# Performance work log

Measured on AMD Instinct MI355X. Metric: run time of the kernel, lower is better.

Reference implementation:

```python
import jax, jax.numpy as jnp
import numpy as np

N = 4096  # n_out = n_in = d_in


def setup_inputs() -> dict:
    key = jax.random.key(0)
    ks = jax.random.split(key, 12)
    f = lambda k, shape: jax.random.normal(k, shape, dtype=jnp.float32)
    center = f(ks[10], (N,))
    radius = jnp.abs(f(ks[11], (N,)))
    return dict(
        W=f(ks[0], (N, N)),
        b=f(ks[1], (N,)),
        prev_W_upper=f(ks[2], (N, N)),
        prev_W_lower=f(ks[3], (N, N)),
        prev_b_upper=f(ks[4], (N,)),
        prev_b_lower=f(ks[5], (N,)),
        prev_W_upper2=f(ks[6], (N, N)),
        prev_W_lower2=f(ks[7], (N, N)),
        prev_b_upper2=f(ks[8], (N,)),
        prev_b_lower2=f(ks[9], (N,)),
        prev_ub=center + radius,
        prev_lb=center - radius,
    )


def reference(W, b, prev_W_upper, prev_W_lower, prev_b_upper, prev_b_lower,
              prev_W_upper2, prev_W_lower2, prev_b_upper2, prev_b_lower2,
              prev_ub, prev_lb):
    # torch: (w_pos * W) @ X + (~w_pos * W) @ Y  ->  W+ @ X + W- @ Y
    Wp = jnp.maximum(W, 0.0)  # W * (W >= 0)
    Wm = jnp.minimum(W, 0.0)  # W * (W <  0)

    # --- forward: compose symbolic bounds with prev layer's ---
    W_upper = Wp @ prev_W_upper + Wm @ prev_W_lower            # [N, N]
    b_upper = Wp @ prev_b_upper + Wm @ prev_b_lower + b        # [N]
    W_lower = Wp @ prev_W_lower + Wm @ prev_W_upper
    b_lower = Wp @ prev_b_lower + Wm @ prev_b_upper + b

    # concretize with W_upper2 = W_lower2 = W, b_upper2 = b_lower2 = b
    ub = Wp @ prev_ub + Wm @ prev_lb + b
    lb = Wp @ prev_lb + Wm @ prev_ub + b

    # --- backsub (prev is the input layer, prev.prev = None -> 1 loop iter) ---
    best_ub, best_lb = ub, lb
    # loop iteration: W_upper = W_lower = W, b_upper = b_lower = b
    ub1 = Wp @ prev_ub + Wm @ prev_lb + b
    lb1 = Wp @ prev_lb + Wm @ prev_ub + b
    best_lb = jnp.maximum(best_lb, lb1)
    best_ub = jnp.minimum(best_ub, ub1)
    bu = Wp @ prev_b_upper2 + Wm @ prev_b_lower2 + b
    bl = Wp @ prev_b_lower2 + Wm @ prev_b_upper2 + b
    Wu = Wp @ prev_W_upper2 + Wm @ prev_W_lower2
    Wl = Wp @ prev_W_lower2 + Wm @ prev_W_upper2
    # final block after loop exit (layer = input layer)
    Wup, Wum = jnp.maximum(Wu, 0.0), jnp.minimum(Wu, 0.0)
    Wlp, Wlm = jnp.maximum(Wl, 0.0), jnp.minimum(Wl, 0.0)
    ub2 = Wup @ prev_ub + Wum @ prev_lb + bu
    lb2 = Wlp @ prev_lb + Wlm @ prev_ub + bl
    best_lb = jnp.maximum(best_lb, lb2)
    best_ub = jnp.minimum(best_ub, ub2)

    bounds = jnp.stack([ub, lb, best_ub, best_lb])  # [4, N]
    return (bounds, W_upper, W_lower, b_upper, b_lower)
```

## Files before the change

kernel.cpp:

```cpp
#include <hip/hip_runtime.h>
#include <hip/hip_bf16.h>
#include <stdint.h>

#define NN 4096

typedef __attribute__((ext_vector_type(8))) short   short8;
typedef __attribute__((ext_vector_type(8))) __bf16  bf16x8;
typedef __attribute__((ext_vector_type(4))) float   f32x4;

__device__ __forceinline__ uint16_t f2bf(float f) {
  uint32_t u = __float_as_uint(f);
  u += 0x7fff + ((u >> 16) & 1);
  return (uint16_t)(u >> 16);
}
__device__ __forceinline__ uint32_t pack2(float a, float b) {
  return (uint32_t)f2bf(a) | ((uint32_t)f2bf(b) << 16);
}

__device__ __forceinline__ void gl_lds16(const void* g, void* l) {
  __builtin_amdgcn_global_load_lds(
      (__attribute__((address_space(1))) void*)g,
      (__attribute__((address_space(3))) void*)l, 16, 0, 0);
}

__global__ __launch_bounds__(256)
void tp_sumdiff(const float* __restrict__ X, const float* __restrict__ Y,
                uint16_t* __restrict__ S, uint16_t* __restrict__ D, int jbase) {
  __shared__ uint16_t sS[64][66];
  __shared__ uint16_t sD[64][66];
  const int t   = threadIdx.x;
  const int j0l = blockIdx.x * 64;
  const int k0  = blockIdx.y * 64;
  const int r   = t >> 2;
  const int c   = (t & 3) * 16;
  const size_t goff = (size_t)(k0 + r) * NN + jbase + j0l + c;
  const float4* px = (const float4*)(X + goff);
  const float4* py = (const float4*)(Y + goff);
#pragma unroll
  for (int i = 0; i < 4; ++i) {
    const float4 vx = px[i];
    const float4 vy = py[i];
    sS[r][c + 4*i]     = f2bf(vx.x + vy.x);
    sS[r][c + 4*i + 1] = f2bf(vx.y + vy.y);
    sS[r][c + 4*i + 2] = f2bf(vx.z + vy.z);
    sS[r][c + 4*i + 3] = f2bf(vx.w + vy.w);
    sD[r][c + 4*i]     = f2bf(vx.x - vy.x);
    sD[r][c + 4*i + 1] = f2bf(vx.y - vy.y);
    sD[r][c + 4*i + 2] = f2bf(vx.z - vy.z);
    sD[r][c + 4*i + 3] = f2bf(vx.w - vy.w);
  }
  __syncthreads();
  const int jj = t >> 2;
  const int kc = (t & 3) * 16;
  uint32_t vs[8], vd[8];
#pragma unroll
  for (int i = 0; i < 8; ++i) {
    vs[i] = (uint32_t)sS[kc + 2*i][jj] | ((uint32_t)sS[kc + 2*i + 1][jj] << 16);
    vd[i] = (uint32_t)sD[kc + 2*i][jj] | ((uint32_t)sD[kc + 2*i + 1][jj] << 16);
  }
  const size_t ooff = (size_t)(j0l + jj) * NN + k0 + kc;
  uint4* ps = (uint4*)(S + ooff);
  uint4* pd = (uint4*)(D + ooff);
  ps[0] = make_uint4(vs[0], vs[1], vs[2], vs[3]);
  ps[1] = make_uint4(vs[4], vs[5], vs[6], vs[7]);
  pd[0] = make_uint4(vd[0], vd[1], vd[2], vd[3]);
  pd[1] = make_uint4(vd[4], vd[5], vd[6], vd[7]);
}

__global__ __launch_bounds__(256)
void wcvt(const float* __restrict__ W, uint16_t* __restrict__ Wb) {
  const size_t base = ((size_t)blockIdx.x * 256 + threadIdx.x) * 8;
  const float4 v0 = *(const float4*)(W + base);
  const float4 v1 = *(const float4*)(W + base + 4);
  *(uint4*)(Wb + base) = make_uint4(pack2(v0.x, v0.y), pack2(v0.z, v0.w),
                                    pack2(v1.x, v1.y), pack2(v1.z, v1.w));
}

__device__ __forceinline__ void epi_write(const f32x4 (&accS)[4][4], const f32x4 (&accD)[4][4],
                                          float* __restrict__ outU, float* __restrict__ outL,
                                          int i0, int j0, int jbase,
                                          int wm, int wn, int lr, int q) {
#pragma unroll
  for (int f = 0; f < 4; ++f)
#pragma unroll
    for (int g = 0; g < 4; ++g) {
      const int col = jbase + j0 + wn + g * 16 + lr;
#pragma unroll
      for (int r = 0; r < 4; ++r) {
        const int row = i0 + wm + f * 16 + q * 4 + r;
        const float s = accS[f][g][r], d = accD[f][g][r];
        outU[(size_t)row * NN + col] = (s + d) * 0.5f;
        outL[(size_t)row * NN + col] = (s - d) * 0.5f;
      }
    }
}

__device__ __forceinline__ void epi_reduce(const f32x4 (&accS)[4][4], const f32x4 (&accD)[4][4],
                                           const float* __restrict__ pub, const float* __restrict__ plb,
                                           float* __restrict__ accUv, float* __restrict__ accLv,
                                           int i0, int j0, int jbase,
                                           int wm, int wn, int lr, int q) {
  float uv[4], lv[4];
#pragma unroll
  for (int g = 0; g < 4; ++g) {
    const int col = jbase + j0 + wn + g * 16 + lr;
    uv[g] = pub[col];
    lv[g] = plb[col];
  }
  float su[16], sl[16];
#pragma unroll
  for (int f = 0; f < 4; ++f)
#pragma unroll
    for (int r = 0; r < 4; ++r) {
      float au = 0.f, al = 0.f;
#pragma unroll
      for (int g = 0; g < 4; ++g) {
        const float s  = accS[f][g][r], d = accD[f][g][r];
        const float wu = (s + d) * 0.5f;
        const float wl = (s - d) * 0.5f;
        au += fmaxf(wu, 0.f) * uv[g] + fminf(wu, 0.f) * lv[g];
        al += fmaxf(wl, 0.f) * lv[g] + fminf(wl, 0.f) * uv[g];
      }
      su[f * 4 + r] = au;
      sl[f * 4 + r] = al;
    }
#pragma unroll
  for (int m = 1; m < 16; m <<= 1)
#pragma unroll
    for (int p = 0; p < 16; ++p) {
      su[p] += __shfl_xor(su[p], m, 64);
      sl[p] += __shfl_xor(sl[p], m, 64);
    }
  const int row = i0 + wm + (lr >> 2) * 16 + q * 4 + (lr & 3);
  atomicAdd(&accUv[row], su[lr]);
  atomicAdd(&accLv[row], sl[lr]);
}

template <int MODE>
__global__ __launch_bounds__(256, 2)
void gemm_bf16(const uint16_t* __restrict__ Ab,
               const uint16_t* __restrict__ Bs,
               const uint16_t* __restrict__ Bd,
               float* __restrict__ outU, float* __restrict__ outL,
               const float* __restrict__ pub, const float* __restrict__ plb,
               float* __restrict__ accUv, float* __restrict__ accLv, int jbase) {
  __shared__ __align__(16) uint16_t sA [128 * 32];
  __shared__ __align__(16) uint16_t sBs[128 * 32];
  __shared__ __align__(16) uint16_t sBd[128 * 32];

  const int tid  = threadIdx.x;
  const int lane = tid & 63;
  const int wv   = tid >> 6;
  const int i0   = blockIdx.y * 128;
  const int j0   = blockIdx.x * 128;
  const int wm   = (wv >> 1) * 64;
  const int wn   = (wv & 1) * 64;
  const int lr   = lane & 15;
  const int q    = lane >> 4;

  f32x4 accS[4][4], accD[4][4];
#pragma unroll
  for (int f = 0; f < 4; ++f)
#pragma unroll
    for (int g = 0; g < 4; ++g) {
      accS[f][g] = f32x4{0.f, 0.f, 0.f, 0.f};
      accD[f][g] = f32x4{0.f, 0.f, 0.f, 0.f};
    }

  const int e0 = tid, e1 = tid + 256;
  const size_t gA0 = (size_t)(i0 + (e0 >> 2)) * NN + (e0 & 3) * 8;
  const size_t gA1 = (size_t)(i0 + (e1 >> 2)) * NN + (e1 & 3) * 8;
  const size_t gB0 = (size_t)(j0 + (e0 >> 2)) * NN + (e0 & 3) * 8;
  const size_t gB1 = (size_t)(j0 + (e1 >> 2)) * NN + (e1 & 3) * 8;

  uint16_t* lA0 = sA  + wv * 512;
  uint16_t* lA1 = sA  + 2048 + wv * 512;
  uint16_t* lS0 = sBs + wv * 512;
  uint16_t* lS1 = sBs + 2048 + wv * 512;
  uint16_t* lD0 = sBd + wv * 512;
  uint16_t* lD1 = sBd + 2048 + wv * 512;

  const short8 msk = {0x7fff,0x7fff,0x7fff,0x7fff,0x7fff,0x7fff,0x7fff,0x7fff};

  for (int kk = 0; kk < NN; kk += 32) {
    __syncthreads();
    gl_lds16(Ab + gA0 + kk, lA0);
    gl_lds16(Ab + gA1 + kk, lA1);
    gl_lds16(Bs + gB0 + kk, lS0);
    gl_lds16(Bs + gB1 + kk, lS1);
    gl_lds16(Bd + gB0 + kk, lD0);
    gl_lds16(Bd + gB1 + kk, lD1);
    __syncthreads();

    bf16x8 a[4], aa[4];
#pragma unroll
    for (int f = 0; f < 4; ++f) {
      short8 as = *(const short8*)(sA + (wm + f * 16 + lr) * 32 + q * 8);
      a[f]  = __builtin_bit_cast(bf16x8, as);
      aa[f] = __builtin_bit_cast(bf16x8, (short8)(as & msk));
    }
#pragma unroll
    for (int g = 0; g < 4; ++g) {
      bf16x8 bs = *(const bf16x8*)(sBs + (wn + g * 16 + lr) * 32 + q * 8);
      bf16x8 bd = *(const bf16x8*)(sBd + (wn + g * 16 + lr) * 32 + q * 8);
#pragma unroll
      for (int f = 0; f < 4; ++f) {
        accS[f][g] = __builtin_amdgcn_mfma_f32_16x16x32_bf16(a[f],  bs, accS[f][g], 0, 0, 0);
        accD[f][g] = __builtin_amdgcn_mfma_f32_16x16x32_bf16(aa[f], bd, accD[f][g], 0, 0, 0);
      }
    }
  }

  if (MODE == 0) {
    epi_write(accS, accD, outU, outL, i0, j0, jbase, wm, wn, lr, q);
  } else {
    epi_reduce(accS, accD, pub, plb, accUv, accLv, i0, j0, jbase, wm, wn, lr, q);
  }
}

template <int MODE>
__global__ __launch_bounds__(256, 2)
void gemm_fused(const float* __restrict__ Wg,
                const uint16_t* __restrict__ Bs,
                const uint16_t* __restrict__ Bd,
                float* __restrict__ outU, float* __restrict__ outL,
                const float* __restrict__ pub, const float* __restrict__ plb,
                float* __restrict__ accUv, float* __restrict__ accLv, int jbase) {
  __shared__ __align__(16) uint16_t sA [128 * 32];
  __shared__ __align__(16) uint16_t sBs[128 * 32];
  __shared__ __align__(16) uint16_t sBd[128 * 32];

  const int tid  = threadIdx.x;
  const int lane = tid & 63;
  const int wv   = tid >> 6;
  const int i0   = blockIdx.y * 128;
  const int j0   = blockIdx.x * 128;
  const int wm   = (wv >> 1) * 64;
  const int wn   = (wv & 1) * 64;
  const int lr   = lane & 15;
  const int q    = lane >> 4;

  f32x4 accS[4][4], accD[4][4];
#pragma unroll
  for (int f = 0; f < 4; ++f)
#pragma unroll
    for (int g = 0; g < 4; ++g) {
      accS[f][g] = f32x4{0.f, 0.f, 0.f, 0.f};
      accD[f][g] = f32x4{0.f, 0.f, 0.f, 0.f};
    }

  const int e0 = tid, e1 = tid + 256;
  const size_t ga0 = (size_t)(i0 + (e0 >> 2)) * NN + (e0 & 3) * 8;
  const size_t ga1 = (size_t)(i0 + (e1 >> 2)) * NN + (e1 & 3) * 8;
  const size_t gb0 = (size_t)(j0 + (e0 >> 2)) * NN + (e0 & 3) * 8;
  const size_t gb1 = (size_t)(j0 + (e1 >> 2)) * NN + (e1 & 3) * 8;

  uint16_t* lS0 = sBs + wv * 512;
  uint16_t* lS1 = sBs + 2048 + wv * 512;
  uint16_t* lD0 = sBd + wv * 512;
  uint16_t* lD1 = sBd + 2048 + wv * 512;

  const short8 msk = {0x7fff,0x7fff,0x7fff,0x7fff,0x7fff,0x7fff,0x7fff,0x7fff};

  for (int kk = 0; kk < NN; kk += 32) {
    const float4 a00 = *(const float4*)(Wg + ga0 + kk);
    const float4 a01 = *(const float4*)(Wg + ga0 + kk + 4);
    const float4 a10 = *(const float4*)(Wg + ga1 + kk);
    const float4 a11 = *(const float4*)(Wg + ga1 + kk + 4);
    const uint4 wA0 = make_uint4(pack2(a00.x, a00.y), pack2(a00.z, a00.w),
                                 pack2(a01.x, a01.y), pack2(a01.z, a01.w));
    const uint4 wA1 = make_uint4(pack2(a10.x, a10.y), pack2(a10.z, a10.w),
                                 pack2(a11.x, a11.y), pack2(a11.z, a11.w));
    __syncthreads();
    gl_lds16(Bs + gb0 + kk, lS0);
    gl_lds16(Bs + gb1 + kk, lS1);
    gl_lds16(Bd + gb0 + kk, lD0);
    gl_lds16(Bd + gb1 + kk, lD1);
    *(uint4*)(sA + e0 * 8) = wA0;
    *(uint4*)(sA + e1 * 8) = wA1;
    __syncthreads();

    bf16x8 a[4], aa[4];
#pragma unroll
    for (int f = 0; f < 4; ++f) {
      short8 as = *(const short8*)(sA + (wm + f * 16 + lr) * 32 + q * 8);
      a[f]  = __builtin_bit_cast(bf16x8, as);
      aa[f] = __builtin_bit_cast(bf16x8, (short8)(as & msk));
    }
#pragma unroll
    for (int g = 0; g < 4; ++g) {
      bf16x8 bs = *(const bf16x8*)(sBs + (wn + g * 16 + lr) * 32 + q * 8);
      bf16x8 bd = *(const bf16x8*)(sBd + (wn + g * 16 + lr) * 32 + q * 8);
#pragma unroll
      for (int f = 0; f < 4; ++f) {
        accS[f][g] = __builtin_amdgcn_mfma_f32_16x16x32_bf16(a[f],  bs, accS[f][g], 0, 0, 0);
        accD[f][g] = __builtin_amdgcn_mfma_f32_16x16x32_bf16(aa[f], bd, accD[f][g], 0, 0, 0);
      }
    }
  }

  if (MODE == 0) {
    epi_write(accS, accD, outU, outL, i0, j0, jbase, wm, wn, lr, q);
  } else {
    epi_reduce(accS, accD, pub, plb, accUv, accLv, i0, j0, jbase, wm, wn, lr, q);
  }
}

__device__ __forceinline__ void load16(const float* p, float* f) {
  const float4* q4 = (const float4*)p;
#pragma unroll
  for (int i = 0; i < 4; ++i) {
    const float4 v = q4[i];
    f[4*i] = v.x; f[4*i+1] = v.y; f[4*i+2] = v.z; f[4*i+3] = v.w;
  }
}

__global__ __launch_bounds__(256)
void matvec6(const float* __restrict__ Wg, const float* __restrict__ bvec,
             const float* __restrict__ pbu,  const float* __restrict__ pbl,
             const float* __restrict__ pbu2, const float* __restrict__ pbl2,
             const float* __restrict__ pub,  const float* __restrict__ plb,
             float* __restrict__ out_bu, float* __restrict__ out_bl,
             float* __restrict__ bounds,
             float* __restrict__ bu_f, float* __restrict__ bl_f) {
  const int row = blockIdx.x;
  const int t   = threadIdx.x;
  const int c0  = t * 16;
  float w[16], xu[16], xl[16], x2u[16], x2l[16], uu[16], ul[16];
  load16(Wg + (size_t)row * NN + c0, w);
  load16(pbu  + c0, xu);  load16(pbl  + c0, xl);
  load16(pbu2 + c0, x2u); load16(pbl2 + c0, x2l);
  load16(pub  + c0, uu);  load16(plb  + c0, ul);
  float a_bu = 0, a_bl = 0, a_ub = 0, a_lb = 0, a_2u = 0, a_2l = 0;
#pragma unroll
  for (int i = 0; i < 16; ++i) {
    const float wp = fmaxf(w[i], 0.f), wm = fminf(w[i], 0.f);
    a_bu += wp * xu[i]  + wm * xl[i];
    a_bl += wp * xl[i]  + wm * xu[i];
    a_ub += wp * uu[i]  + wm * ul[i];
    a_lb += wp * ul[i]  + wm * uu[i];
    a_2u += wp * x2u[i] + wm * x2l[i];
    a_2l += wp * x2l[i] + wm * x2u[i];
  }
#pragma unroll
  for (int off = 32; off; off >>= 1) {
    a_bu += __shfl_down(a_bu, off, 64);
    a_bl += __shfl_down(a_bl, off, 64);
    a_ub += __shfl_down(a_ub, off, 64);
    a_lb += __shfl_down(a_lb, off, 64);
    a_2u += __shfl_down(a_2u, off, 64);
    a_2l += __shfl_down(a_2l, off, 64);
  }
  __shared__ float red[4][6];
  const int lane = t & 63, wvv = t >> 6;
  if (lane == 0) {
    red[wvv][0] = a_bu; red[wvv][1] = a_bl; red[wvv][2] = a_ub;
    red[wvv][3] = a_lb; red[wvv][4] = a_2u; red[wvv][5] = a_2l;
  }
  __syncthreads();
  if (t == 0) {
    float r0=0, r1=0, r2=0, r3=0, r4=0, r5=0;
    for (int v = 0; v < 4; ++v) {
      r0 += red[v][0]; r1 += red[v][1]; r2 += red[v][2];
      r3 += red[v][3]; r4 += red[v][4]; r5 += red[v][5];
    }
    const float bb = bvec[row];
    out_bu[row]      = r0 + bb;
    out_bl[row]      = r1 + bb;
    bounds[row]      = r2 + bb;
    bounds[NN + row] = r3 + bb;
    bu_f[row]        = r4 + bb;
    bl_f[row]        = r5 + bb;
  }
}

__global__ __launch_bounds__(256)
void finalize_bounds(const float* __restrict__ accU, const float* __restrict__ accL,
                     const float* __restrict__ bu_f, const float* __restrict__ bl_f,
                     float* __restrict__ bounds) {
  const int i = blockIdx.x * 256 + threadIdx.x;
  if (i >= NN) return;
  const float ub  = bounds[i];
  const float lb  = bounds[NN + i];
  const float ub2 = accU[i] + bu_f[i];
  const float lb2 = accL[i] + bl_f[i];
  bounds[2 * NN + i] = fminf(ub, ub2);
  bounds[3 * NN + i] = fmaxf(lb, lb2);
}

extern "C" void kernel_launch(void* const* d_in, const int* in_sizes, int n_in,
                              void* d_out, int out_size, void* d_ws, size_t ws_size,
                              hipStream_t stream) {
  const float* W    = (const float*)d_in[0];
  const float* b    = (const float*)d_in[1];
  const float* pWu  = (const float*)d_in[2];
  const float* pWl  = (const float*)d_in[3];
  const float* pbu  = (const float*)d_in[4];
  const float* pbl  = (const float*)d_in[5];
  const float* pWu2 = (const float*)d_in[6];
  const float* pWl2 = (const float*)d_in[7];
  const float* pbu2 = (const float*)d_in[8];
  const float* pbl2 = (const float*)d_in[9];
  const float* pub  = (const float*)d_in[10];
  const float* plb  = (const float*)d_in[11];

  float* out    = (float*)d_out;
  float* bounds = out;
  float* Wup    = out + 4 * NN;
  float* Wlo    = Wup + (size_t)NN * NN;
  float* b_up   = Wlo + (size_t)NN * NN;
  float* b_lo   = b_up + NN;

  float* accU = (float*)d_ws;
  float* accL = accU + NN;
  float* bu_f = accL + NN;
  float* bl_f = bu_f + NN;
  const size_t hdr = 65536;
  const size_t WBF = (size_t)NN * NN;

  (void)hipMemsetAsync(accU, 0, 2 * NN * sizeof(float), stream);

  int Pf = 1;
  while (Pf < 32 && hdr + 2 * WBF + 2 * ((size_t)NN / Pf) * NN * 2 > ws_size) Pf *= 2;
  const bool fast = (hdr + 2 * WBF + 2 * ((size_t)NN / Pf) * NN * 2 <= ws_size);

  if (fast) {
    uint16_t* Wbf = (uint16_t*)((char*)d_ws + hdr);
    const int NPf = NN / Pf;
    uint16_t* Sp = Wbf + WBF;
    uint16_t* Dp = Sp + (size_t)NPf * NN;

    wcvt<<<dim3(8192), 256, 0, stream>>>(W, Wbf);

    tp_sumdiff<<<dim3(64, 64), 256, 0, stream>>>(pWu2, pWl2,
                                                 (uint16_t*)Wup, (uint16_t*)Wlo, 0);
    gemm_bf16<1><<<dim3(32, 32), 256, 0, stream>>>(Wbf, (uint16_t*)Wup, (uint16_t*)Wlo,
                                                   nullptr, nullptr,
                                                   pub, plb, accU, accL, 0);

    for (int p = 0; p < Pf; ++p) {
      const int jb = p * NPf;
      tp_sumdiff<<<dim3(NPf / 64, 64), 256, 0, stream>>>(pWu, pWl, Sp, Dp, jb);
      gemm_bf16<0><<<dim3(NPf / 128, 32), 256, 0, stream>>>(Wbf, Sp, Dp, Wup, Wlo,
                                                            nullptr, nullptr,
                                                            nullptr, nullptr, jb);
    }
  } else {
    int P = 1;
    while (P < 32 && hdr + 2 * ((size_t)NN / P) * NN * 2 > ws_size) P *= 2;
    const int NP = NN / P;
    uint16_t* big = (uint16_t*)((char*)d_ws + hdr);
    uint16_t* Sp = big;
    uint16_t* Dp = big + (size_t)NP * NN;

    tp_sumdiff<<<dim3(64, 64), 256, 0, stream>>>(pWu2, pWl2,
                                                 (uint16_t*)Wup, (uint16_t*)Wlo, 0);
    gemm_fused<1><<<dim3(32, 32), 256, 0, stream>>>(W, (uint16_t*)Wup, (uint16_t*)Wlo,
                                                    nullptr, nullptr,
                                                    pub, plb, accU, accL, 0);
    for (int p = 0; p < P; ++p) {
      const int jb = p * NP;
      tp_sumdiff<<<dim3(NP / 64, 64), 256, 0, stream>>>(pWu, pWl, Sp, Dp, jb);
      gemm_fused<0><<<dim3(NP / 128, 32), 256, 0, stream>>>(W, Sp, Dp, Wup, Wlo,
                                                            nullptr, nullptr,
                                                            nullptr, nullptr, jb);
    }
  }

  matvec6<<<NN, 256, 0, stream>>>(W, b, pbu, pbl, pbu2, pbl2, pub, plb,
                                  b_up, b_lo, bounds, bu_f, bl_f);
  finalize_bounds<<<16, 256, 0, stream>>>(accU, accL, bu_f, bl_f, bounds);
}
```

Baseline: 991.1 us.

## Replace bf16 GEMM with 8-wave 4-stage pipelined kernel and XCD-aware tile remap

Swaps the single-buffered 256-thread GEMM for a 512-thread kernel with 256x128 tiles. It uses a 4-slot LDS ring with 3-deep prefetch via global_load_lds, explicit vmcnt waits and barriers, and MFMA phases that run at raised priority. Block IDs are remapped so consecutive tiles land on the same XCD to improve L2 reuse. The aim is to hide global-load latency and remove the two full syncthreads per k-step, at the cost of 128KB of LDS and fragile hand-written waitcnt logic.

```diff
diff --git a/kernel.cpp b/kernel.cpp
--- a/kernel.cpp
+++ b/kernel.cpp
@@ -137,26 +137,30 @@
 }
 
 template <int MODE>
-__global__ __launch_bounds__(256, 2)
-void gemm_bf16(const uint16_t* __restrict__ Ab,
-               const uint16_t* __restrict__ Bs,
-               const uint16_t* __restrict__ Bd,
-               float* __restrict__ outU, float* __restrict__ outL,
-               const float* __restrict__ pub, const float* __restrict__ plb,
-               float* __restrict__ accUv, float* __restrict__ accLv, int jbase) {
-  __shared__ __align__(16) uint16_t sA [128 * 32];
-  __shared__ __align__(16) uint16_t sBs[128 * 32];
-  __shared__ __align__(16) uint16_t sBd[128 * 32];
+__global__ __launch_bounds__(512, 2)
+void gemm8p(const uint16_t* __restrict__ Ab,
+            const uint16_t* __restrict__ Bs,
+            const uint16_t* __restrict__ Bd,
+            float* __restrict__ outU, float* __restrict__ outL,
+            const float* __restrict__ pub, const float* __restrict__ plb,
+            float* __restrict__ accUv, float* __restrict__ accLv, int jbase) {
+  __shared__ __align__(16) uint16_t sm[4 * 16384];
 
   const int tid  = threadIdx.x;
   const int lane = tid & 63;
   const int wv   = tid >> 6;
-  const int i0   = blockIdx.y * 128;
-  const int j0   = blockIdx.x * 128;
-  const int wm   = (wv >> 1) * 64;
-  const int wn   = (wv & 1) * 64;
-  const int lr   = lane & 15;
-  const int q    = lane >> 4;
+
+  const int gx  = (int)gridDim.x;
+  const int nwg = gx * (int)gridDim.y;
+  const int raw = (int)blockIdx.y * gx + (int)blockIdx.x;
+  const int id  = (raw & 7) * (nwg >> 3) + (raw >> 3);
+  const int i0  = (id / gx) * 256;
+  const int j0  = (id % gx) * 128;
+
+  const int wm = (wv >> 1) * 64;
+  const int wn = (wv & 1) * 64;
+  const int lr = lane & 15;
+  const int q  = lane >> 4;
 
   f32x4 accS[4][4], accD[4][4];
 #pragma unroll
@@ -167,48 +171,84 @@
       accD[f][g] = f32x4{0.f, 0.f, 0.f, 0.f};
     }
 
-  const int e0 = tid, e1 = tid + 256;
-  const size_t gA0 = (size_t)(i0 + (e0 >> 2)) * NN + (e0 & 3) * 8;
-  const size_t gA1 = (size_t)(i0 + (e1 >> 2)) * NN + (e1 & 3) * 8;
-  const size_t gB0 = (size_t)(j0 + (e0 >> 2)) * NN + (e0 & 3) * 8;
-  const size_t gB1 = (size_t)(j0 + (e1 >> 2)) * NN + (e1 & 3) * 8;
-
-  uint16_t* lA0 = sA  + wv * 512;
-  uint16_t* lA1 = sA  + 2048 + wv * 512;
-  uint16_t* lS0 = sBs + wv * 512;
-  uint16_t* lS1 = sBs + 2048 + wv * 512;
-  uint16_t* lD0 = sBd + wv * 512;
-  uint16_t* lD1 = sBd + 2048 + wv * 512;
+  const uint32_t colc = (uint32_t)(tid & 3) * 8;
+  const uint32_t rA0  = (uint32_t)(i0 + (tid >> 2)) * NN + colc;
+  const uint32_t rA1  = rA0 + 128u * NN;
+  const uint32_t rB   = (uint32_t)(j0 + (tid >> 2)) * NN + colc;
+
+  const int lA0 = wv * 512;
+  const int lA1 = 4096  + wv * 512;
+  const int lBs = 8192  + wv * 512;
+  const int lBd = 12288 + wv * 512;
 
   const short8 msk = {0x7fff,0x7fff,0x7fff,0x7fff,0x7fff,0x7fff,0x7fff,0x7fff};
 
-  for (int kk = 0; kk < NN; kk += 32) {
-    __syncthreads();
-    gl_lds16(Ab + gA0 + kk, lA0);
-    gl_lds16(Ab + gA1 + kk, lA1);
-    gl_lds16(Bs + gB0 + kk, lS0);
-    gl_lds16(Bs + gB1 + kk, lS1);
-    gl_lds16(Bd + gB0 + kk, lD0);
-    gl_lds16(Bd + gB1 + kk, lD1);
-    __syncthreads();
-
-    bf16x8 a[4], aa[4];
-#pragma unroll
-    for (int f = 0; f < 4; ++f) {
-      short8 as = *(const short8*)(sA + (wm + f * 16 + lr) * 32 + q * 8);
-      a[f]  = __builtin_bit_cast(bf16x8, as);
-      aa[f] = __builtin_bit_cast(bf16x8, (short8)(as & msk));
-    }
-#pragma unroll
-    for (int g = 0; g < 4; ++g) {
-      bf16x8 bs = *(const bf16x8*)(sBs + (wn + g * 16 + lr) * 32 + q * 8);
-      bf16x8 bd = *(const bf16x8*)(sBd + (wn + g * 16 + lr) * 32 + q * 8);
-#pragma unroll
-      for (int f = 0; f < 4; ++f) {
-        accS[f][g] = __builtin_amdgcn_mfma_f32_16x16x32_bf16(a[f],  bs, accS[f][g], 0, 0, 0);
-        accD[f][g] = __builtin_amdgcn_mfma_f32_16x16x32_bf16(aa[f], bd, accD[f][g], 0, 0, 0);
-      }
-    }
+#pragma unroll
+  for (int t0 = 0; t0 < 3; ++t0) {
+    uint16_t* ns = sm + t0 * 16384;
+    const uint32_t kn = (uint32_t)t0 * 32;
+    gl_lds16(Ab + rA0 + kn, ns + lA0);
+    gl_lds16(Ab + rA1 + kn, ns + lA1);
+    gl_lds16(Bs + rB  + kn, ns + lBs);
+    gl_lds16(Bd + rB  + kn, ns + lBd);
+  }
+  asm volatile("s_waitcnt vmcnt(8)" ::: "memory");
+  asm volatile("s_barrier" ::: "memory");
+
+  for (int t = 0; t < 128; ++t) {
+    const uint16_t* sl = sm + (t & 3) * 16384;
+    const bool pf = (t + 3 < 128);
+    uint16_t* ns = sm + ((t + 3) & 3) * 16384;
+    const uint32_t kn = (uint32_t)(t + 3) * 32;
+
+    bf16x8 a[4], bsf[4];
+#pragma unroll
+    for (int f = 0; f < 4; ++f)
+      a[f] = __builtin_bit_cast(bf16x8,
+             *(const short8*)(sl + (wm + f * 16 + lr) * 32 + q * 8));
+#pragma unroll
+    for (int g = 0; g < 4; ++g)
+      bsf[g] = __builtin_bit_cast(bf16x8,
+               *(const short8*)(sl + 8192 + (wn + g * 16 + lr) * 32 + q * 8));
+    if (pf) {
+      gl_lds16(Ab + rA0 + kn, ns + lA0);
+      gl_lds16(Ab + rA1 + kn, ns + lA1);
+    }
+    asm volatile("s_barrier" ::: "memory");
+    __builtin_amdgcn_s_setprio(1);
+#pragma unroll
+    for (int g = 0; g < 4; ++g)
+#pragma unroll
+      for (int f = 0; f < 4; ++f)
+        accS[f][g] = __builtin_amdgcn_mfma_f32_16x16x32_bf16(a[f], bsf[g], accS[f][g], 0, 0, 0);
+    __builtin_amdgcn_s_setprio(0);
+    asm volatile("s_barrier" ::: "memory");
+
+    bf16x8 aa[4], bdf[4];
+#pragma unroll
+    for (int f = 0; f < 4; ++f)
+      aa[f] = __builtin_bit_cast(bf16x8,
+              (short8)(__builtin_bit_cast(short8, a[f]) & msk));
+#pragma unroll
+    for (int g = 0; g < 4; ++g)
+      bdf[g] = __builtin_bit_cast(bf16x8,
+               *(const short8*)(sl + 12288 + (wn + g * 16 + lr) * 32 + q * 8));
+    if (pf) {
+      gl_lds16(Bs + rB + kn, ns + lBs);
+      gl_lds16(Bd + rB + kn, ns + lBd);
+    }
+    if (pf)            asm volatile("s_waitcnt vmcnt(8)" ::: "memory");
+    else if (t == 125) asm volatile("s_waitcnt vmcnt(4)" ::: "memory");
+    else if (t == 126) asm volatile("s_waitcnt vmcnt(0)" ::: "memory");
+    asm volatile("s_barrier" ::: "memory");
+    __builtin_amdgcn_s_setprio(1);
+#pragma unroll
+    for (int g = 0; g < 4; ++g)
+#pragma unroll
+      for (int f = 0; f < 4; ++f)
+        accD[f][g] = __builtin_amdgcn_mfma_f32_16x16x32_bf16(aa[f], bdf[g], accD[f][g], 0, 0, 0);
+    __builtin_amdgcn_s_setprio(0);
+    asm volatile("s_barrier" ::: "memory");
   }
 
   if (MODE == 0) {
@@ -434,16 +474,16 @@
 
     tp_sumdiff<<<dim3(64, 64), 256, 0, stream>>>(pWu2, pWl2,
                                                  (uint16_t*)Wup, (uint16_t*)Wlo, 0);
-    gemm_bf16<1><<<dim3(32, 32), 256, 0, stream>>>(Wbf, (uint16_t*)Wup, (uint16_t*)Wlo,
-                                                   nullptr, nullptr,
-                                                   pub, plb, accU, accL, 0);
+    gemm8p<1><<<dim3(32, 16), 512, 0, stream>>>(Wbf, (uint16_t*)Wup, (uint16_t*)Wlo,
+                                                nullptr, nullptr,
+                                                pub, plb, accU, accL, 0);
 
     for (int p = 0; p < Pf; ++p) {
       const int jb = p * NPf;
       tp_sumdiff<<<dim3(NPf / 64, 64), 256, 0, stream>>>(pWu, pWl, Sp, Dp, jb);
-      gemm_bf16<0><<<dim3(NPf / 128, 32), 256, 0, stream>>>(Wbf, Sp, Dp, Wup, Wlo,
-                                                            nullptr, nullptr,
-                                                            nullptr, nullptr, jb);
+      gemm8p<0><<<dim3(NPf / 128, 16), 512, 0, stream>>>(Wbf, Sp, Dp, Wup, Wlo,
+                                                         nullptr, nullptr,
+                                                         nullptr, nullptr, jb);
     }
   } else {
     int P = 1;
```

Result: no change. 996.6 us (+0.6%).
